# Optimization experiments

Hardware: AMD Instinct MI355X
Metric: run time of the kernel (lower is better)

## Reference

```python
import jax, jax.numpy as jnp
import numpy as np

B, C, L = 256, 512, 150
CI = C // 4            # channel_in = in_dim // 4 = 128
K = 150                # one_hot_cls_num (depthwise kernel over length)
POOL = 150             # MaxPool2d kernel (150, 1)
EPS = 1e-5             # BatchNorm eps


def setup_inputs() -> dict:
    key = jax.random.key(0)
    ks = jax.random.split(key, 8)
    n = lambda k, shape, s: jax.random.normal(k, shape, jnp.float32) * s
    return {
        "x":    jax.random.normal(ks[0], (B, C, L, 1), jnp.float32),
        "Wv":   n(ks[1], (CI, C), 0.06),   "bv": jnp.zeros((CI,), jnp.float32),
        "Wq":   n(ks[2], (CI, CI), 0.12),  "bq": jnp.zeros((CI,), jnp.float32),
        "Wk":   n(ks[3], (CI, CI), 0.12),  "bk": jnp.zeros((CI,), jnp.float32),
        "gamma": n(ks[4], (), 1.0),
        "Wd":   n(ks[5], (2 * CI, K), 0.1), "bd": jnp.zeros((2 * CI,), jnp.float32),
        "Wp":   n(ks[6], (2 * CI, 2 * CI), 0.08), "bp": jnp.zeros((2 * CI,), jnp.float32),
        "bn_g": jnp.ones((2 * CI,), jnp.float32),
        "bn_b": jnp.zeros((2 * CI,), jnp.float32),
    }


def reference(x, Wv, bv, Wq, bq, Wk, bk, gamma, Wd, bd, Wp, bp, bn_g, bn_b):
    xb = x[..., 0]                                             # [B, C, L] (trailing width==1)
    # 1x1 convs are per-position matmuls over the channel dim
    v = jnp.einsum('oc,bcl->bol', Wv, xb) + bv[:, None]        # [B, CI, L]
    q = jnp.einsum('oc,bcl->bol', Wq, v) + bq[:, None]         # [B, CI, L]
    k = jnp.einsum('oc,bcl->bol', Wk, v) + bk[:, None]         # [B, CI, L]
    # raw (unscaled) attention: energy = q^T k, softmax over keys
    energy = jnp.einsum('bci,bcj->bij', q, k)                  # [B, L, L]
    attn = jax.nn.softmax(energy, axis=-1)
    # x = bmm(v, attn^T): out[b,c,i] = sum_j v[b,c,j] * attn[b,i,j]
    att_out = jnp.einsum('bcj,bij->bci', v, attn)              # [B, CI, L]
    cat = jnp.concatenate([gamma * att_out, v], axis=1)        # [B, 2CI, L]
    # MaxPool2d kernel=(150,1), stride=(150,1) over length
    Lp = L // POOL
    y = cat[:, :, : Lp * POOL].reshape(B, 2 * CI, Lp, POOL).max(axis=-1)
    y = y.reshape(B, -1)                                       # [B, 2CI*Lp]
    # depthwise conv kernel (K,1), VALID padding, groups = 2CI
    dw = jax.lax.conv_general_dilated(
        cat[:, :, :, None],                                    # [B, 2CI, L, 1]
        Wd[:, None, :, None],                                  # [2CI, 1, K, 1]
        window_strides=(1, 1), padding='VALID',
        dimension_numbers=('NCHW', 'OIHW', 'NCHW'),
        feature_group_count=2 * CI,
    ) + bd[None, :, None, None]                                # [B, 2CI, L-K+1, 1]
    # pointwise 1x1 conv
    pw = jnp.einsum('oc,bchw->bohw', Wp, dw) + bp[None, :, None, None]
    # BatchNorm2d in training mode: per-channel batch stats (biased variance)
    mean = pw.mean(axis=(0, 2, 3))
    var = pw.var(axis=(0, 2, 3))
    xn = (pw - mean[None, :, None, None]) * jax.lax.rsqrt(var[None, :, None, None] + EPS)
    out = jax.nn.relu(xn * bn_g[None, :, None, None] + bn_b[None, :, None, None])
    return jnp.concatenate([out.reshape(B, -1), y], axis=1)    # [B, 2CI*(L-K+1) + 2CI*Lp]
```

## Files before the change

kernel.cpp:

```cpp
#include <hip/hip_runtime.h>


typedef float f32x4 __attribute__((ext_vector_type(4)));
typedef short s16x8 __attribute__((ext_vector_type(8)));
typedef unsigned short BF;

union U8 { s16x8 v; BF u[8]; uint2 d[2]; };

__device__ __forceinline__ BF bfhi(float f) { return (BF)(__float_as_uint(f) >> 16); }
__device__ __forceinline__ float bff(BF h) { return __uint_as_float(((unsigned)h) << 16); }
__device__ __forceinline__ BF bflo(float f, BF hi) { return bfhi(f - bff(hi)); }
__device__ __forceinline__ BF bfrne(float f) {
    unsigned u = __float_as_uint(f);
    u += 0x7fffu + ((u >> 16) & 1u);
    return (BF)(u >> 16);
}
__device__ __forceinline__ s16x8 ld8l(const BF* p) {
    U8 t; t.d[0] = *(const uint2*)p; t.d[1] = *(const uint2*)(p + 4); return t.v;
}
__device__ __forceinline__ void st4(BF* p, BF a, BF b, BF c, BF d) {
    uint2 t; t.x = (unsigned)a | ((unsigned)b << 16);
    t.y = (unsigned)c | ((unsigned)d << 16);
    *(uint2*)p = t;
}
#define MFMA(a, b, c) __builtin_amdgcn_mfma_f32_16x16x32_bf16(a, b, c, 0, 0, 0)

__global__ __launch_bounds__(256)
void prep_all(const float* __restrict__ Wv, const float* __restrict__ Wq,
              const float* __restrict__ Wk, const float* __restrict__ bq,
              BF* __restrict__ wvh, BF* __restrict__ wvl,
              BF* __restrict__ wqh, BF* __restrict__ wql,
              float* __restrict__ cvec)
{
    __shared__ float qs[128][33], ks_[128][33];
    const int blk = blockIdx.x, tid = threadIdx.x;
    if (blk < 64) {
        int i = blk * 1024 + tid * 4;
        float4 v = *(const float4*)(Wv + i);
        BF h0 = bfhi(v.x), h1 = bfhi(v.y), h2 = bfhi(v.z), h3 = bfhi(v.w);
        st4(&wvh[i], h0, h1, h2, h3);
        st4(&wvl[i], bflo(v.x,h0), bflo(v.y,h1), bflo(v.z,h2), bflo(v.w,h3));
    } else if (blk < 80) {
        int bi = blk - 64;
        int d1_0 = (bi >> 2) * 32, d2_0 = (bi & 3) * 32;
        for (int i = tid; i < 4096; i += 256) {
            int o = i >> 5, c = i & 31;
            qs[o][c]  = Wq[o * 128 + d1_0 + c];
            ks_[o][c] = Wk[o * 128 + d2_0 + c];
        }
        __syncthreads();
        #pragma unroll
        for (int j = 0; j < 4; ++j) {
            int idx = j * 256 + tid;
            int d1 = idx >> 5, d2 = idx & 31;
            float s = 0.f;
            #pragma unroll 8
            for (int o = 0; o < 128; ++o) s = fmaf(qs[o][d1], ks_[o][d2], s);
            BF h = bfhi(s);
            wqh[(d1_0 + d1) * 128 + d2_0 + d2] = h;
            wql[(d1_0 + d1) * 128 + d2_0 + d2] = bflo(s, h);
        }
    } else {
        if (tid < 128) {
            float s = 0.f;
            for (int o = 0; o < 128; ++o) s += bq[o] * Wk[o * 128 + tid];
            cvec[tid] = s;
        }
    }
}

__global__ __launch_bounds__(1024, 4)
void fused_attn(const float* __restrict__ x, const BF* __restrict__ wvh,
                const BF* __restrict__ wvl, const float* __restrict__ bv,
                const BF* __restrict__ wqh, const BF* __restrict__ wql,
                const float* __restrict__ cvec, const float* __restrict__ gammap,
                const float* __restrict__ Wd, float* __restrict__ dw,
                float* __restrict__ out)
{
    __shared__ char smem[149504];
    BF (*vh)[140] = (BF(*)[140])smem;
    BF (*vl)[140] = (BF(*)[140])(smem + 44800);
    BF (*xt)[160][68] = (BF(*)[160][68])(smem + 89600);
    BF (*ts)[2][192][36] = (BF(*)[2][192][36])(smem + 89600);
    BF (*P)[172] = (BF(*)[172])(smem + 44800);
    float* smax = (float*)(smem + 144896);
    float* ssum = smax + 480;
    float* svec = ssum + 480;

    const int b = blockIdx.x;
    const float* xb = x + (long)b * 76800;
    const int tid = threadIdx.x;
    const int lane = tid & 63, w = tid >> 6;
    const int li = lane & 15, gq = lane >> 4;
    const float gamma = gammap[0];

    {
        const int wm = w & 1, wn = w >> 1;
        f32x4 acc[5];
        #pragma unroll
        for (int i = 0; i < 5; ++i) acc[i] = f32x4{0.f,0.f,0.f,0.f};

        {
            float cur[3][4];
            #pragma unroll
            for (int it = 0; it < 3; ++it) {
                int l = it * 64 + lane;
                #pragma unroll
                for (int cc = 0; cc < 4; ++cc)
                    cur[it][cc] = (l < 150) ? xb[(w * 4 + cc) * 150 + l] : 0.f;
            }
            #pragma unroll
            for (int it = 0; it < 3; ++it) {
                int l = it * 64 + lane;
                if (l < 160) {
                    BF h0=bfhi(cur[it][0]), h1=bfhi(cur[it][1]), h2=bfhi(cur[it][2]), h3=bfhi(cur[it][3]);
                    st4(&xt[0][l][w * 4], h0, h1, h2, h3);
                    st4(&xt[1][l][w * 4], bflo(cur[it][0],h0), bflo(cur[it][1],h1),
                                          bflo(cur[it][2],h2), bflo(cur[it][3],h3));
                }
            }
        }
        __syncthreads();

        for (int p = 0; p < 8; ++p) {
            float nxt[3][4];
            if (p < 7) {
                #pragma unroll
                for (int it = 0; it < 3; ++it) {
                    int l = it * 64 + lane;
                    #pragma unroll
                    for (int cc = 0; cc < 4; ++cc)
                        nxt[it][cc] = (l < 150) ? xb[((p+1)*64 + w*4 + cc) * 150 + l] : 0.f;
                }
            }
            s16x8 bhv[2], blv[2];
            #pragma unroll
            for (int kd = 0; kd < 2; ++kd) {
                long g = (long)(wn * 16 + li) * 512 + p * 64 + kd * 32 + gq * 8;
                bhv[kd] = *(const s16x8*)(wvh + g);
                blv[kd] = *(const s16x8*)(wvl + g);
            }
            #pragma unroll
            for (int kd = 0; kd < 2; ++kd) {
                #pragma unroll
                for (int mf = 0; mf < 5; ++mf) {
                    int row = wm * 80 + mf * 16 + li, col = kd * 32 + gq * 8;
                    s16x8 ah = ld8l(&xt[0][row][col]);
                    s16x8 al = ld8l(&xt[1][row][col]);
                    acc[mf] = MFMA(ah, bhv[kd], acc[mf]);
                    acc[mf] = MFMA(ah, blv[kd], acc[mf]);
                    acc[mf] = MFMA(al, bhv[kd], acc[mf]);
                }
            }
            __syncthreads();
            if (p < 7) {
                #pragma unroll
                for (int it = 0; it < 3; ++it) {
                    int l = it * 64 + lane;
                    if (l < 160) {
                        BF h0=bfhi(nxt[it][0]), h1=bfhi(nxt[it][1]), h2=bfhi(nxt[it][2]), h3=bfhi(nxt[it][3]);
                        st4(&xt[0][l][w * 4], h0, h1, h2, h3);
                        st4(&xt[1][l][w * 4], bflo(nxt[it][0],h0), bflo(nxt[it][1],h1),
                                              bflo(nxt[it][2],h2), bflo(nxt[it][3],h3));
                    }
                }
            }
            __syncthreads();
        }

        {
            int c = wn * 16 + li;
            float bvv = bv[c];
            #pragma unroll
            for (int mf = 0; mf < 5; ++mf)
                #pragma unroll
                for (int r = 0; r < 4; ++r) {
                    int l = wm * 80 + mf * 16 + gq * 4 + r;
                    float f = acc[mf][r] + bvv;
                    BF h = bfhi(f);
                    vh[l][c] = h;
                    vl[l][c] = bflo(f, h);
                }
        }
    }
    __syncthreads();

    if (tid < 640) {
        int j = tid >> 2, q3 = tid & 3;
        float s = 0.f;
        #pragma unroll 8
        for (int d2 = q3 * 32; d2 < q3 * 32 + 32; ++d2)
            s += cvec[d2] * bff(vh[j][d2]);
        s += __shfl_xor(s, 1); s += __shfl_xor(s, 2);
        if (q3 == 0) svec[j] = s;
    } else if (tid < 672) {
        svec[160 + (tid - 640)] = 0.f;
    }
    __syncthreads();

    f32x4 eacc[2][4];
    #pragma unroll
    for (int a = 0; a < 2; ++a)
        #pragma unroll
        for (int b2 = 0; b2 < 4; ++b2) eacc[a][b2] = f32x4{0.f,0.f,0.f,0.f};
    const int iw = w / 3, jw = w % 3;

    for (int pr = 0; pr < 2; ++pr) {
        if (w < 8) {
            int ss  = pr * 2 + ((w >> 2) & 1);
            int tjj = w & 1, tcc = (w >> 1) & 1;
            f32x4 tacc[5];
            #pragma unroll
            for (int i = 0; i < 5; ++i) tacc[i] = f32x4{0.f,0.f,0.f,0.f};
            int c = ss * 32 + tcc * 16 + li;
            #pragma unroll
            for (int kd = 0; kd < 4; ++kd) {
                long go = (long)c * 128 + kd * 32 + gq * 8;
                s16x8 bh = *(const s16x8*)(wqh + go);
                s16x8 bl = *(const s16x8*)(wql + go);
                #pragma unroll
                for (int mf = 0; mf < 5; ++mf) {
                    int row = tjj * 80 + mf * 16 + li, col = kd * 32 + gq * 8;
                    s16x8 ah = ld8l(&vh[row][col]);
                    s16x8 al = ld8l(&vl[row][col]);
                    tacc[mf] = MFMA(ah, bh, tacc[mf]);
                    tacc[mf] = MFMA(ah, bl, tacc[mf]);
                    tacc[mf] = MFMA(al, bh, tacc[mf]);
                }
            }
            #pragma unroll
            for (int mf = 0; mf < 5; ++mf)
                #pragma unroll
                for (int r = 0; r < 4; ++r) {
                    int j = tjj * 80 + mf * 16 + gq * 4 + r;
                    int cp = tcc * 16 + li;
                    float f = tacc[mf][r];
                    BF h = bfhi(f);
                    ts[ss & 1][0][j][cp] = h;
                    ts[ss & 1][1][j][cp] = bflo(f, h);
                }
        }
        __syncthreads();
        if (w < 15) {
            #pragma unroll
            for (int s2 = 0; s2 < 2; ++s2) {
                int scol = (pr * 2 + s2) * 32 + gq * 8;
                s16x8 ah[2], al[2];
                #pragma unroll
                for (int mf2 = 0; mf2 < 2; ++mf2) {
                    int row = iw * 32 + mf2 * 16 + li;
                    ah[mf2] = ld8l(&vh[row][scol]);
                    al[mf2] = ld8l(&vl[row][scol]);
                }
                #pragma unroll
                for (int nf = 0; nf < 4; ++nf) {
                    int jr = jw * 64 + nf * 16 + li;
                    s16x8 bh = ld8l(&ts[s2][0][jr][gq * 8]);
                    s16x8 bl = ld8l(&ts[s2][1][jr][gq * 8]);
                    #pragma unroll
                    for (int mf2 = 0; mf2 < 2; ++mf2) {
                        eacc[mf2][nf] = MFMA(ah[mf2], bh, eacc[mf2][nf]);
                        eacc[mf2][nf] = MFMA(ah[mf2], bl, eacc[mf2][nf]);
                        eacc[mf2][nf] = MFMA(al[mf2], bh, eacc[mf2][nf]);
                    }
                }
            }
        }
        __syncthreads();
    }

    if (w < 15) {
        #pragma unroll
        for (int nf = 0; nf < 4; ++nf) {
            int j = jw * 64 + nf * 16 + li;
            float sv = svec[j];
            #pragma unroll
            for (int mf2 = 0; mf2 < 2; ++mf2)
                #pragma unroll
                for (int r = 0; r < 4; ++r)
                    eacc[mf2][nf][r] += sv;
        }
        #pragma unroll
        for (int mf2 = 0; mf2 < 2; ++mf2)
            #pragma unroll
            for (int r = 0; r < 4; ++r) {
                int i = iw * 32 + mf2 * 16 + gq * 4 + r;
                float m = -3.4e38f;
                #pragma unroll
                for (int nf = 0; nf < 4; ++nf) {
                    int j = jw * 64 + nf * 16 + li;
                    if (j < 150) m = fmaxf(m, eacc[mf2][nf][r]);
                }
                #pragma unroll
                for (int o = 1; o < 16; o <<= 1) m = fmaxf(m, __shfl_xor(m, o));
                if (li == 0) smax[jw * 160 + i] = m;
            }
    }
    __syncthreads();
    if (w < 15) {
        #pragma unroll
        for (int mf2 = 0; mf2 < 2; ++mf2)
            #pragma unroll
            for (int r = 0; r < 4; ++r) {
                int i = iw * 32 + mf2 * 16 + gq * 4 + r;
                float gm = fmaxf(fmaxf(smax[i], smax[160 + i]), smax[320 + i]);
                float rs_ = 0.f;
                #pragma unroll
                for (int nf = 0; nf < 4; ++nf) {
                    int j = jw * 64 + nf * 16 + li;
                    float e = (j < 150) ? __expf(eacc[mf2][nf][r] - gm) : 0.f;
                    eacc[mf2][nf][r] = e;
                    rs_ += e;
                }
                #pragma unroll
                for (int o = 1; o < 16; o <<= 1) rs_ += __shfl_xor(rs_, o);
                if (li == 0) ssum[jw * 160 + i] = rs_;
            }
    }
    __syncthreads();
    if (w < 15) {
        #pragma unroll
        for (int mf2 = 0; mf2 < 2; ++mf2)
            #pragma unroll
            for (int r = 0; r < 4; ++r) {
                int i = iw * 32 + mf2 * 16 + gq * 4 + r;
                float inv = 1.f / (ssum[i] + ssum[160 + i] + ssum[320 + i]);
                #pragma unroll
                for (int nf = 0; nf < 4; ++nf) {
                    int j = jw * 64 + nf * 16 + li;
                    if (j < 160) P[i][j] = bfrne(eacc[mf2][nf][r] * inv);
                }
            }
    }
    __syncthreads();

    {
        const int pc = w & 7, pi = w >> 3;
        f32x4 oacc[5];
        #pragma unroll
        for (int i = 0; i < 5; ++i) oacc[i] = f32x4{0.f,0.f,0.f,0.f};
        #pragma unroll
        for (int ks = 0; ks < 5; ++ks) {
            int c = pc * 16 + li;
            int j0 = ks * 32 + gq * 8;
            U8 t;
            #pragma unroll
            for (int e = 0; e < 8; ++e) t.u[e] = vh[j0 + e][c];
            #pragma unroll
            for (int nf2 = 0; nf2 < 5; ++nf2) {
                int ir = pi * 80 + nf2 * 16 + li;
                s16x8 bp = ld8l(&P[ir][ks * 32 + gq * 8]);
                oacc[nf2] = MFMA(t.v, bp, oacc[nf2]);
            }
        }

        float* pmax = smax;
        float* pdot = ssum;
        #pragma unroll
        for (int r = 0; r < 4; ++r) {
            int c = pc * 16 + gq * 4 + r;
            float mx = -3.4e38f, dt = 0.f;
            #pragma unroll
            for (int nf2 = 0; nf2 < 5; ++nf2) {
                int l = pi * 80 + nf2 * 16 + li;
                if (l < 150) {
                    float val = gamma * oacc[nf2][r];
                    mx = fmaxf(mx, val);
                    dt = fmaf(val, Wd[c * 150 + l], dt);
                }
            }
            #pragma unroll
            for (int o = 1; o < 16; o <<= 1) {
                mx = fmaxf(mx, __shfl_xor(mx, o));
                dt += __shfl_xor(dt, o);
            }
            if (li == 0) { pmax[pi * 128 + c] = mx; pdot[pi * 128 + c] = dt; }
        }
        __syncthreads();
        if (tid < 128) {
            out[(long)b * 512 + 256 + tid] = fmaxf(pmax[tid], pmax[128 + tid]);
            dw[b * 256 + tid] = pdot[tid] + pdot[128 + tid];
        } else if (tid >= 256 && tid < 768) {
            int t2 = tid - 256, c2 = t2 >> 2, q3 = t2 & 3;
            const int st[5] = {0, 37, 75, 112, 150};
            float mx = -3.4e38f, dt = 0.f;
            for (int l = st[q3]; l < st[q3 + 1]; ++l) {
                float val = bff(vh[l][c2]);
                mx = fmaxf(mx, val);
                dt = fmaf(val, Wd[(128 + c2) * 150 + l], dt);
            }
            mx = fmaxf(mx, __shfl_xor(mx, 1));
            dt += __shfl_xor(dt, 1);
            mx = fmaxf(mx, __shfl_xor(mx, 2));
            dt += __shfl_xor(dt, 2);
            if (q3 == 0) {
                out[(long)b * 512 + 256 + 128 + c2] = mx;
                dw[b * 256 + 128 + c2] = dt;
            }
        }
    }
}

__global__ __launch_bounds__(256)
void tail_pwbn(const float* __restrict__ dw, const float* __restrict__ Wp,
               const float* __restrict__ bn_g, const float* __restrict__ bn_b,
               float* __restrict__ out)
{
    __shared__ float wp_s[256];
    __shared__ float rs[4], rs2[4];
    const int o = blockIdx.x, t = threadIdx.x;
    const int lane = t & 63, w = t >> 6;
    wp_s[t] = Wp[o * 256 + t];
    __syncthreads();
    const float4* dr = (const float4*)(dw + (long)t * 256);
    float acc = 0.f;
    #pragma unroll 8
    for (int i = 0; i < 64; ++i) {
        float4 d4 = dr[i];
        acc = fmaf(d4.x, wp_s[i*4+0], acc);
        acc = fmaf(d4.y, wp_s[i*4+1], acc);
        acc = fmaf(d4.z, wp_s[i*4+2], acc);
        acc = fmaf(d4.w, wp_s[i*4+3], acc);
    }
    float s = acc, s2 = acc * acc;
    #pragma unroll
    for (int d = 1; d < 64; d <<= 1) { s += __shfl_xor(s, d); s2 += __shfl_xor(s2, d); }
    if (lane == 0) { rs[w] = s; rs2[w] = s2; }
    __syncthreads();
    float S  = rs[0] + rs[1] + rs[2] + rs[3];
    float S2 = rs2[0] + rs2[1] + rs2[2] + rs2[3];
    float mean = S * (1.f/256.f);
    float var  = S2 * (1.f/256.f) - mean * mean;
    float sc = rsqrtf(var + 1e-5f) * bn_g[o];
    float sh = bn_b[o] - mean * sc;
    out[(long)t * 512 + o] = fmaxf(fmaf(acc, sc, sh), 0.f);
}

extern "C" void kernel_launch(void* const* d_in, const int* in_sizes, int n_in,
                              void* d_out, int out_size, void* d_ws, size_t ws_size,
                              hipStream_t stream)
{
    (void)in_sizes; (void)n_in; (void)out_size; (void)ws_size;
    const float* x    = (const float*)d_in[0];
    const float* Wv   = (const float*)d_in[1];
    const float* bv   = (const float*)d_in[2];
    const float* Wq   = (const float*)d_in[3];
    const float* bq   = (const float*)d_in[4];
    const float* Wk   = (const float*)d_in[5];
    const float* bk   = (const float*)d_in[6];  (void)bk;
    const float* gam  = (const float*)d_in[7];
    const float* Wd   = (const float*)d_in[8];
    const float* Wp   = (const float*)d_in[10];
    const float* bn_g = (const float*)d_in[12];
    const float* bn_b = (const float*)d_in[13];
    float* out = (float*)d_out;

    char* wsb = (char*)d_ws;
    BF* wvh  = (BF*)wsb;
    BF* wvl  = (BF*)(wsb + 131072);
    BF* wqh  = (BF*)(wsb + 262144);
    BF* wql  = (BF*)(wsb + 294912);
    float* cvec = (float*)(wsb + 327680);
    float* dw   = (float*)(wsb + 328192);

    prep_all<<<81, 256, 0, stream>>>(Wv, Wq, Wk, bq, wvh, wvl, wqh, wql, cvec);
    fused_attn<<<256, 1024, 0, stream>>>(x, wvh, wvl, bv, wqh, wql, cvec,
                                         gam, Wd, dw, out);
    tail_pwbn<<<256, 256, 0, stream>>>(dw, Wp, bn_g, bn_b, out);
}
```

Before: 95.18 us.

## Warp-specialize V projection with producer warps and double-buffered x chunks

The V projection phase now splits the block into 8 compute warps that run MFMAs over 32-channel k-chunks with register-prefetched weights, and 8 producer warps that load and split x into a double-buffered shared-memory tile. The Q^T K transform moves to 32x32x16 MFMAs on 10 warps, while the remaining warps compute the bias vector dot products in parallel. The goal is to overlap global loads of x with matrix work and to cut the number of barriers per channel. In exchange only half the warps do MFMA work in the first phase, and shared memory use grows slightly.

New measurement: 88.51 us. -7.0%, faster.

```diff
diff --git a/kernel.cpp b/kernel.cpp
--- a/kernel.cpp
+++ b/kernel.cpp
@@ -1,8 +1,9 @@
 #include <hip/hip_runtime.h>
 
 
-typedef float f32x4 __attribute__((ext_vector_type(4)));
-typedef short s16x8 __attribute__((ext_vector_type(8)));
+typedef float f32x4  __attribute__((ext_vector_type(4)));
+typedef float f32x16 __attribute__((ext_vector_type(16)));
+typedef short s16x8  __attribute__((ext_vector_type(8)));
 typedef unsigned short BF;
 
 union U8 { s16x8 v; BF u[8]; uint2 d[2]; };
@@ -23,7 +24,8 @@
     t.y = (unsigned)c | ((unsigned)d << 16);
     *(uint2*)p = t;
 }
-#define MFMA(a, b, c) __builtin_amdgcn_mfma_f32_16x16x32_bf16(a, b, c, 0, 0, 0)
+#define MFMA(a, b, c)   __builtin_amdgcn_mfma_f32_16x16x32_bf16(a, b, c, 0, 0, 0)
+#define MFMA32(a, b, c) __builtin_amdgcn_mfma_f32_32x32x16_bf16(a, b, c, 0, 0, 0)
 
 __global__ __launch_bounds__(256)
 void prep_all(const float* __restrict__ Wv, const float* __restrict__ Wq,
@@ -77,15 +79,15 @@
                 const float* __restrict__ Wd, float* __restrict__ dw,
                 float* __restrict__ out)
 {
-    __shared__ char smem[149504];
+    __shared__ char smem[150272];
     BF (*vh)[140] = (BF(*)[140])smem;
     BF (*vl)[140] = (BF(*)[140])(smem + 44800);
-    BF (*xt)[160][68] = (BF(*)[160][68])(smem + 89600);
+    BF (*xt)[2][160][36] = (BF(*)[2][160][36])(smem + 89600);
     BF (*ts)[2][192][36] = (BF(*)[2][192][36])(smem + 89600);
     BF (*P)[172] = (BF(*)[172])(smem + 44800);
     float* smax = (float*)(smem + 144896);
     float* ssum = smax + 480;
-    float* svec = ssum + 480;
+    float* svp  = ssum + 480;
 
     const int b = blockIdx.x;
     const float* xb = x + (long)b * 76800;
@@ -94,107 +96,100 @@
     const int li = lane & 15, gq = lane >> 4;
     const float gamma = gammap[0];
 
-    {
+    if (w < 8) {
         const int wm = w & 1, wn = w >> 1;
-        f32x4 acc[5];
-        #pragma unroll
-        for (int i = 0; i < 5; ++i) acc[i] = f32x4{0.f,0.f,0.f,0.f};
-
-        {
-            float cur[3][4];
-            #pragma unroll
-            for (int it = 0; it < 3; ++it) {
-                int l = it * 64 + lane;
-                #pragma unroll
-                for (int cc = 0; cc < 4; ++cc)
-                    cur[it][cc] = (l < 150) ? xb[(w * 4 + cc) * 150 + l] : 0.f;
-            }
-            #pragma unroll
-            for (int it = 0; it < 3; ++it) {
-                int l = it * 64 + lane;
-                if (l < 160) {
-                    BF h0=bfhi(cur[it][0]), h1=bfhi(cur[it][1]), h2=bfhi(cur[it][2]), h3=bfhi(cur[it][3]);
-                    st4(&xt[0][l][w * 4], h0, h1, h2, h3);
-                    st4(&xt[1][l][w * 4], bflo(cur[it][0],h0), bflo(cur[it][1],h1),
-                                          bflo(cur[it][2],h2), bflo(cur[it][3],h3));
-                }
-            }
-        }
-        __syncthreads();
-
-        for (int p = 0; p < 8; ++p) {
-            float nxt[3][4];
-            if (p < 7) {
-                #pragma unroll
-                for (int it = 0; it < 3; ++it) {
-                    int l = it * 64 + lane;
-                    #pragma unroll
-                    for (int cc = 0; cc < 4; ++cc)
-                        nxt[it][cc] = (l < 150) ? xb[((p+1)*64 + w*4 + cc) * 150 + l] : 0.f;
-                }
-            }
-            s16x8 bhv[2], blv[2];
-            #pragma unroll
-            for (int kd = 0; kd < 2; ++kd) {
-                long g = (long)(wn * 16 + li) * 512 + p * 64 + kd * 32 + gq * 8;
-                bhv[kd] = *(const s16x8*)(wvh + g);
-                blv[kd] = *(const s16x8*)(wvl + g);
-            }
-            #pragma unroll
-            for (int kd = 0; kd < 2; ++kd) {
-                #pragma unroll
-                for (int mf = 0; mf < 5; ++mf) {
-                    int row = wm * 80 + mf * 16 + li, col = kd * 32 + gq * 8;
-                    s16x8 ah = ld8l(&xt[0][row][col]);
-                    s16x8 al = ld8l(&xt[1][row][col]);
-                    acc[mf] = MFMA(ah, bhv[kd], acc[mf]);
-                    acc[mf] = MFMA(ah, blv[kd], acc[mf]);
-                    acc[mf] = MFMA(al, bhv[kd], acc[mf]);
-                }
+        f32x4 acc[5][2];
+        #pragma unroll
+        for (int mf = 0; mf < 5; ++mf)
+            #pragma unroll
+            for (int nf = 0; nf < 2; ++nf) acc[mf][nf] = f32x4{0.f,0.f,0.f,0.f};
+        s16x8 bh[2], bl[2];
+        #pragma unroll
+        for (int nf = 0; nf < 2; ++nf) {
+            long g = (long)(wn*32 + nf*16 + li)*512 + gq*8;
+            bh[nf] = *(const s16x8*)(wvh + g);
+            bl[nf] = *(const s16x8*)(wvl + g);
+        }
+        __syncthreads();
+        for (int p = 0; p < 16; ++p) {
+            s16x8 nbh[2], nbl[2];
+            if (p < 15) {
+                #pragma unroll
+                for (int nf = 0; nf < 2; ++nf) {
+                    long g = (long)(wn*32 + nf*16 + li)*512 + (p+1)*32 + gq*8;
+                    nbh[nf] = *(const s16x8*)(wvh + g);
+                    nbl[nf] = *(const s16x8*)(wvl + g);
+                }
+            }
+            const BF (*xh)[36]  = xt[p & 1][0];
+            const BF (*xl2)[36] = xt[p & 1][1];
+            #pragma unroll
+            for (int mf = 0; mf < 5; ++mf) {
+                int row = wm*80 + mf*16 + li;
+                s16x8 ah = ld8l(&xh[row][gq*8]);
+                s16x8 al = ld8l(&xl2[row][gq*8]);
+                #pragma unroll
+                for (int nf = 0; nf < 2; ++nf) {
+                    acc[mf][nf] = MFMA(al, bh[nf], acc[mf][nf]);
+                    acc[mf][nf] = MFMA(ah, bl[nf], acc[mf][nf]);
+                    acc[mf][nf] = MFMA(ah, bh[nf], acc[mf][nf]);
+                }
+            }
+            if (p < 15) {
+                #pragma unroll
+                for (int nf = 0; nf < 2; ++nf) { bh[nf] = nbh[nf]; bl[nf] = nbl[nf]; }
             }
             __syncthreads();
-            if (p < 7) {
-                #pragma unroll
-                for (int it = 0; it < 3; ++it) {
-                    int l = it * 64 + lane;
-                    if (l < 160) {
-                        BF h0=bfhi(nxt[it][0]), h1=bfhi(nxt[it][1]), h2=bfhi(nxt[it][2]), h3=bfhi(nxt[it][3]);
-                        st4(&xt[0][l][w * 4], h0, h1, h2, h3);
-                        st4(&xt[1][l][w * 4], bflo(nxt[it][0],h0), bflo(nxt[it][1],h1),
-                                              bflo(nxt[it][2],h2), bflo(nxt[it][3],h3));
-                    }
-                }
-            }
-            __syncthreads();
-        }
-
-        {
-            int c = wn * 16 + li;
+        }
+        #pragma unroll
+        for (int nf = 0; nf < 2; ++nf) {
+            int c = wn*32 + nf*16 + li;
             float bvv = bv[c];
             #pragma unroll
             for (int mf = 0; mf < 5; ++mf)
                 #pragma unroll
                 for (int r = 0; r < 4; ++r) {
-                    int l = wm * 80 + mf * 16 + gq * 4 + r;
-                    float f = acc[mf][r] + bvv;
+                    int l = wm*80 + mf*16 + gq*4 + r;
+                    float f = acc[mf][nf][r] + bvv;
                     BF h = bfhi(f);
                     vh[l][c] = h;
                     vl[l][c] = bflo(f, h);
                 }
         }
-    }
-    __syncthreads();
-
-    if (tid < 640) {
-        int j = tid >> 2, q3 = tid & 3;
-        float s = 0.f;
-        #pragma unroll 8
-        for (int d2 = q3 * 32; d2 < q3 * 32 + 32; ++d2)
-            s += cvec[d2] * bff(vh[j][d2]);
-        s += __shfl_xor(s, 1); s += __shfl_xor(s, 2);
-        if (q3 == 0) svec[j] = s;
-    } else if (tid < 672) {
-        svec[160 + (tid - 640)] = 0.f;
+    } else {
+        const int sw = w - 8;
+        float cur[3][4];
+        auto ldchunk = [&](int p) {
+            #pragma unroll
+            for (int it = 0; it < 3; ++it) {
+                int l = it*64 + lane;
+                #pragma unroll
+                for (int cc = 0; cc < 4; ++cc)
+                    cur[it][cc] = (l < 150) ? xb[(p*32 + sw*4 + cc)*150 + l] : 0.f;
+            }
+        };
+        auto wrchunk = [&](int buf) {
+            #pragma unroll
+            for (int it = 0; it < 3; ++it) {
+                int l = it*64 + lane;
+                if (l < 160) {
+                    BF h0=bfhi(cur[it][0]), h1=bfhi(cur[it][1]);
+                    BF h2=bfhi(cur[it][2]), h3=bfhi(cur[it][3]);
+                    st4(&xt[buf][0][l][sw*4], h0, h1, h2, h3);
+                    st4(&xt[buf][1][l][sw*4], bflo(cur[it][0],h0), bflo(cur[it][1],h1),
+                                              bflo(cur[it][2],h2), bflo(cur[it][3],h3));
+                }
+            }
+        };
+        ldchunk(0); wrchunk(0); ldchunk(1);
+        __syncthreads();
+        for (int p = 0; p < 16; ++p) {
+            if (p < 15) {
+                wrchunk((p + 1) & 1);
+                if (p < 14) ldchunk(p + 2);
+            }
+            __syncthreads();
+        }
     }
     __syncthreads();
 
@@ -204,59 +199,64 @@
         #pragma unroll
         for (int b2 = 0; b2 < 4; ++b2) eacc[a][b2] = f32x4{0.f,0.f,0.f,0.f};
     const int iw = w / 3, jw = w % 3;
+    const int l31 = lane & 31, hi5 = lane >> 5;
 
     for (int pr = 0; pr < 2; ++pr) {
-        if (w < 8) {
-            int ss  = pr * 2 + ((w >> 2) & 1);
-            int tjj = w & 1, tcc = (w >> 1) & 1;
-            f32x4 tacc[5];
-            #pragma unroll
-            for (int i = 0; i < 5; ++i) tacc[i] = f32x4{0.f,0.f,0.f,0.f};
-            int c = ss * 32 + tcc * 16 + li;
-            #pragma unroll
-            for (int kd = 0; kd < 4; ++kd) {
-                long go = (long)c * 128 + kd * 32 + gq * 8;
-                s16x8 bh = *(const s16x8*)(wqh + go);
-                s16x8 bl = *(const s16x8*)(wql + go);
-                #pragma unroll
-                for (int mf = 0; mf < 5; ++mf) {
-                    int row = tjj * 80 + mf * 16 + li, col = kd * 32 + gq * 8;
-                    s16x8 ah = ld8l(&vh[row][col]);
-                    s16x8 al = ld8l(&vl[row][col]);
-                    tacc[mf] = MFMA(ah, bh, tacc[mf]);
-                    tacc[mf] = MFMA(ah, bl, tacc[mf]);
-                    tacc[mf] = MFMA(al, bh, tacc[mf]);
-                }
-            }
-            #pragma unroll
-            for (int mf = 0; mf < 5; ++mf)
-                #pragma unroll
-                for (int r = 0; r < 4; ++r) {
-                    int j = tjj * 80 + mf * 16 + gq * 4 + r;
-                    int cp = tcc * 16 + li;
-                    float f = tacc[mf][r];
-                    BF h = bfhi(f);
-                    ts[ss & 1][0][j][cp] = h;
-                    ts[ss & 1][1][j][cp] = bflo(f, h);
-                }
+        if (w < 10) {
+            const int s2 = w / 5, jt = w % 5;
+            const int ss = pr*2 + s2;
+            f32x16 tacc;
+            #pragma unroll
+            for (int r = 0; r < 16; ++r) tacc[r] = 0.f;
+            const int cg2 = ss*32 + l31;
+            const int jr0 = jt*32 + l31;
+            #pragma unroll
+            for (int kc = 0; kc < 8; ++kc) {
+                int kof = kc*16 + hi5*8;
+                s16x8 bh = *(const s16x8*)(wqh + (long)cg2*128 + kof);
+                s16x8 bl = *(const s16x8*)(wql + (long)cg2*128 + kof);
+                s16x8 ah = ld8l(&vh[jr0][kof]);
+                s16x8 al = ld8l(&vl[jr0][kof]);
+                tacc = MFMA32(al, bh, tacc);
+                tacc = MFMA32(ah, bl, tacc);
+                tacc = MFMA32(ah, bh, tacc);
+            }
+            #pragma unroll
+            for (int r = 0; r < 16; ++r) {
+                int j = jt*32 + (r & 3) + 8*(r >> 2) + 4*hi5;
+                float f = tacc[r];
+                BF h = bfhi(f);
+                ts[s2][0][j][l31] = h;
+                ts[s2][1][j][l31] = bflo(f, h);
+            }
+        } else if (pr == 0) {
+            int t2 = tid - 640;
+            int r = t2 >> 1, hf = t2 & 1;
+            if (r < 160) {
+                float s = 0.f;
+                #pragma unroll 8
+                for (int d2 = hf*64; d2 < hf*64 + 64; ++d2)
+                    s += cvec[d2] * bff(vh[r][d2]);
+                svp[hf*192 + r] = s;
+            }
         }
         __syncthreads();
         if (w < 15) {
             #pragma unroll
             for (int s2 = 0; s2 < 2; ++s2) {
-                int scol = (pr * 2 + s2) * 32 + gq * 8;
+                int scol = (pr*2 + s2)*32 + gq*8;
                 s16x8 ah[2], al[2];
                 #pragma unroll
                 for (int mf2 = 0; mf2 < 2; ++mf2) {
-                    int row = iw * 32 + mf2 * 16 + li;
+                    int row = iw*32 + mf2*16 + li;
                     ah[mf2] = ld8l(&vh[row][scol]);
                     al[mf2] = ld8l(&vl[row][scol]);
                 }
                 #pragma unroll
                 for (int nf = 0; nf < 4; ++nf) {
-                    int jr = jw * 64 + nf * 16 + li;
-                    s16x8 bh = ld8l(&ts[s2][0][jr][gq * 8]);
-                    s16x8 bl = ld8l(&ts[s2][1][jr][gq * 8]);
+                    int jr = jw*64 + nf*16 + li;
+                    s16x8 bh = ld8l(&ts[s2][0][jr][gq*8]);
+                    s16x8 bl = ld8l(&ts[s2][1][jr][gq*8]);
                     #pragma unroll
                     for (int mf2 = 0; mf2 < 2; ++mf2) {
                         eacc[mf2][nf] = MFMA(ah[mf2], bh, eacc[mf2][nf]);
@@ -272,8 +272,8 @@
     if (w < 15) {
         #pragma unroll
         for (int nf = 0; nf < 4; ++nf) {
-            int j = jw * 64 + nf * 16 + li;
-            float sv = svec[j];
+            int j = jw*64 + nf*16 + li;
+            float sv = svp[j] + svp[192 + j];
             #pragma unroll
             for (int mf2 = 0; mf2 < 2; ++mf2)
                 #pragma unroll
@@ -284,16 +284,16 @@
         for (int mf2 = 0; mf2 < 2; ++mf2)
             #pragma unroll
             for (int r = 0; r < 4; ++r) {
-                int i = iw * 32 + mf2 * 16 + gq * 4 + r;
+                int i = iw*32 + mf2*16 + gq*4 + r;
                 float m = -3.4e38f;
                 #pragma unroll
                 for (int nf = 0; nf < 4; ++nf) {
-                    int j = jw * 64 + nf * 16 + li;
+                    int j = jw*64 + nf*16 + li;
                     if (j < 150) m = fmaxf(m, eacc[mf2][nf][r]);
                 }
                 #pragma unroll
                 for (int o = 1; o < 16; o <<= 1) m = fmaxf(m, __shfl_xor(m, o));
-                if (li == 0) smax[jw * 160 + i] = m;
+                if (li == 0) smax[jw*160 + i] = m;
             }
     }
     __syncthreads();
@@ -302,19 +302,19 @@
         for (int mf2 = 0; mf2 < 2; ++mf2)
             #pragma unroll
             for (int r = 0; r < 4; ++r) {
-                int i = iw * 32 + mf2 * 16 + gq * 4 + r;
+                int i = iw*32 + mf2*16 + gq*4 + r;
                 float gm = fmaxf(fmaxf(smax[i], smax[160 + i]), smax[320 + i]);
                 float rs_ = 0.f;
                 #pragma unroll
                 for (int nf = 0; nf < 4; ++nf) {
-                    int j = jw * 64 + nf * 16 + li;
+                    int j = jw*64 + nf*16 + li;
                     float e = (j < 150) ? __expf(eacc[mf2][nf][r] - gm) : 0.f;
                     eacc[mf2][nf][r] = e;
                     rs_ += e;
                 }
                 #pragma unroll
                 for (int o = 1; o < 16; o <<= 1) rs_ += __shfl_xor(rs_, o);
-                if (li == 0) ssum[jw * 160 + i] = rs_;
+                if (li == 0) ssum[jw*160 + i] = rs_;
             }
     }
     __syncthreads();
@@ -323,11 +323,11 @@
         for (int mf2 = 0; mf2 < 2; ++mf2)
             #pragma unroll
             for (int r = 0; r < 4; ++r) {
-                int i = iw * 32 + mf2 * 16 + gq * 4 + r;
+                int i = iw*32 + mf2*16 + gq*4 + r;
                 float inv = 1.f / (ssum[i] + ssum[160 + i] + ssum[320 + i]);
                 #pragma unroll
                 for (int nf = 0; nf < 4; ++nf) {
-                    int j = jw * 64 + nf * 16 + li;
+                    int j = jw*64 + nf*16 + li;
                     if (j < 160) P[i][j] = bfrne(eacc[mf2][nf][r] * inv);
                 }
             }
@@ -341,15 +341,15 @@
         for (int i = 0; i < 5; ++i) oacc[i] = f32x4{0.f,0.f,0.f,0.f};
         #pragma unroll
         for (int ks = 0; ks < 5; ++ks) {
-            int c = pc * 16 + li;
-            int j0 = ks * 32 + gq * 8;
+            int c = pc*16 + li;
+            int j0 = ks*32 + gq*8;
             U8 t;
             #pragma unroll
             for (int e = 0; e < 8; ++e) t.u[e] = vh[j0 + e][c];
             #pragma unroll
             for (int nf2 = 0; nf2 < 5; ++nf2) {
-                int ir = pi * 80 + nf2 * 16 + li;
-                s16x8 bp = ld8l(&P[ir][ks * 32 + gq * 8]);
+                int ir = pi*80 + nf2*16 + li;
+                s16x8 bp = ld8l(&P[ir][ks*32 + gq*8]);
                 oacc[nf2] = MFMA(t.v, bp, oacc[nf2]);
             }
         }
@@ -358,15 +358,15 @@
         float* pdot = ssum;
         #pragma unroll
         for (int r = 0; r < 4; ++r) {
-            int c = pc * 16 + gq * 4 + r;
+            int c = pc*16 + gq*4 + r;
             float mx = -3.4e38f, dt = 0.f;
             #pragma unroll
             for (int nf2 = 0; nf2 < 5; ++nf2) {
-                int l = pi * 80 + nf2 * 16 + li;
+                int l = pi*80 + nf2*16 + li;
                 if (l < 150) {
                     float val = gamma * oacc[nf2][r];
                     mx = fmaxf(mx, val);
-                    dt = fmaf(val, Wd[c * 150 + l], dt);
+                    dt = fmaf(val, Wd[c*150 + l], dt);
                 }
             }
             #pragma unroll
@@ -374,28 +374,28 @@
                 mx = fmaxf(mx, __shfl_xor(mx, o));
                 dt += __shfl_xor(dt, o);
             }
-            if (li == 0) { pmax[pi * 128 + c] = mx; pdot[pi * 128 + c] = dt; }
+            if (li == 0) { pmax[pi*128 + c] = mx; pdot[pi*128 + c] = dt; }
         }
         __syncthreads();
         if (tid < 128) {
-            out[(long)b * 512 + 256 + tid] = fmaxf(pmax[tid], pmax[128 + tid]);
-            dw[b * 256 + tid] = pdot[tid] + pdot[128 + tid];
+            out[(long)b*512 + 256 + tid] = fmaxf(pmax[tid], pmax[128 + tid]);
+            dw[b*256 + tid] = pdot[tid] + pdot[128 + tid];
         } else if (tid >= 256 && tid < 768) {
             int t2 = tid - 256, c2 = t2 >> 2, q3 = t2 & 3;
-            const int st[5] = {0, 37, 75, 112, 150};
+            int l0 = (q3*150) >> 2, l1 = ((q3 + 1)*150) >> 2;
             float mx = -3.4e38f, dt = 0.f;
-            for (int l = st[q3]; l < st[q3 + 1]; ++l) {
+            for (int l = l0; l < l1; ++l) {
                 float val = bff(vh[l][c2]);
                 mx = fmaxf(mx, val);
-                dt = fmaf(val, Wd[(128 + c2) * 150 + l], dt);
+                dt = fmaf(val, Wd[(128 + c2)*150 + l], dt);
             }
             mx = fmaxf(mx, __shfl_xor(mx, 1));
             dt += __shfl_xor(dt, 1);
             mx = fmaxf(mx, __shfl_xor(mx, 2));
             dt += __shfl_xor(dt, 2);
             if (q3 == 0) {
-                out[(long)b * 512 + 256 + 128 + c2] = mx;
-                dw[b * 256 + 128 + c2] = dt;
+                out[(long)b*512 + 256 + 128 + c2] = mx;
+                dw[b*256 + 128 + c2] = dt;
             }
         }
     }
```
